# Optimization experiments

Hardware: AMD Instinct MI355X
Metric: run time of the kernel (lower is better)

The kernel has to match this reference:

```python
import jax, jax.numpy as jnp
import numpy as np

TOP_K = 4


def setup_inputs() -> dict:
    key = jax.random.key(0)
    k1, k2, k3 = jax.random.split(key, 3)
    tokens, hidden_dim, num_experts = 16384, 2880, 128
    hidden_states = jax.random.normal(k1, (tokens, hidden_dim), dtype=jnp.float32)
    weight = jax.random.normal(k2, (num_experts, hidden_dim), dtype=jnp.float32) * 0.02
    bias = jax.random.normal(k3, (num_experts,), dtype=jnp.float32) * 0.02
    return {"hidden_states": hidden_states, "weight": weight, "bias": bias}


def reference(hidden_states, weight, bias):
    # hidden_states: [T, H]; weight: [E, H]; bias: [E]
    x = hidden_states.reshape(-1, weight.shape[1])
    router_logits = jnp.einsum("th,eh->te", x, weight) + bias  # [T, E]
    router_top_value, router_indices = jax.lax.top_k(router_logits, TOP_K)  # [T, K]
    router_top_value = jax.nn.softmax(router_top_value, axis=-1)
    return router_top_value, router_indices, router_logits
```

## Files before the change

kernel.cpp:

```cpp
#include <hip/hip_runtime.h>
#include <math.h>

#define H       2880
#define H4      720
#define NTOK    16384
#define NEXP    128
#define NCHUNK  90
#define NSTEP   180
#define GAP_EPS 1e-3f

typedef __attribute__((ext_vector_type(8)))  short bf16x8;
typedef __attribute__((ext_vector_type(16))) float f32x16;

union FragU { unsigned int u[4]; bf16x8 v; };

__device__ inline bf16x8 pack_hi2(float4 a, float4 b) {
    const float f[8] = {a.x,a.y,a.z,a.w,b.x,b.y,b.z,b.w};
    FragU r;
#pragma unroll
    for (int j = 0; j < 4; ++j) {
        unsigned u0 = __float_as_uint(f[2*j]);
        unsigned u1 = __float_as_uint(f[2*j+1]);
        r.u[j] = (u1 & 0xFFFF0000u) | (u0 >> 16);
    }
    return r.v;
}
__device__ inline bf16x8 pack_lo2(float4 a, float4 b) {
    const float f[8] = {a.x,a.y,a.z,a.w,b.x,b.y,b.z,b.w};
    FragU r;
#pragma unroll
    for (int j = 0; j < 4; ++j) {
        float x0 = f[2*j],   h0 = __uint_as_float(__float_as_uint(x0) & 0xFFFF0000u);
        float x1 = f[2*j+1], h1 = __uint_as_float(__float_as_uint(x1) & 0xFFFF0000u);
        unsigned l0 = __float_as_uint(x0 - h0);
        unsigned l1 = __float_as_uint(x1 - h1);
        r.u[j] = (l1 & 0xFFFF0000u) | (l0 >> 16);
    }
    return r.v;
}

__global__ __launch_bounds__(256) void wconv(
    const float* __restrict__ w, short* __restrict__ whiF, short* __restrict__ wloF)
{
    const int gid = blockIdx.x * 256 + threadIdx.x;
    const int l   = gid & 63;
    const int nt  = (gid >> 6) & 3;
    const int s   = gid >> 8;
    const int e   = nt * 32 + (l & 31);
    const int k0  = s * 16 + (l >> 5) * 8;
    const float4* wp = (const float4*)(w + (size_t)e * H + k0);
    const float4 a = wp[0], b = wp[1];
    *(bf16x8*)(whiF + (size_t)gid * 8) = pack_hi2(a, b);
    *(bf16x8*)(wloF + (size_t)gid * 8) = pack_lo2(a, b);
}

__global__ __launch_bounds__(64, 2) void router_gemm_mfma(
    const float* __restrict__ x,
    const short* __restrict__ whiF,
    const short* __restrict__ wloF,
    float* __restrict__ p0,
    float* __restrict__ pws)
{
    __shared__ float xs[3][1024];

    const int lane = threadIdx.x;
    const int bm   = blockIdx.x;
    const int z    = blockIdx.y;
    const int ks   = gridDim.y;
    const int t0   = bm * 32;

    const int base = NCHUNK / ks, rem = NCHUNK % ks;
    const int c0 = z * base + (z < rem ? z : rem);
    const int c1 = c0 + base + (z < rem ? 1 : 0);

    float* outp = (z == 0) ? p0 : (pws + (size_t)(z - 1) * NTOK * NEXP);

    const float4* gs = (const float4*)x + (size_t)(t0 + (lane >> 3)) * H4 + ((lane & 7) ^ (lane >> 3));
    const unsigned xsb = (unsigned)(uintptr_t)&xs[0][0];
    const int r31 = lane & 31, lx7 = lane & 7, kh2 = (lane >> 5) * 2;

    f32x16 acc[4];
#pragma unroll
    for (int nt = 0; nt < 4; ++nt)
#pragma unroll
        for (int r = 0; r < 16; ++r) acc[nt][r] = 0.0f;

    bf16x8 bc[16], bn[16];

#define GL(SRC, DST) __builtin_amdgcn_global_load_lds(                                   \
        (const __attribute__((address_space(1))) void*)(SRC),                            \
        (__attribute__((address_space(3))) void*)(DST), 16, 0, 0)

#define STAGE(SB, CC) {                                                                  \
    const float4* g_ = gs + (size_t)(CC) * 8;                                            \
    GL(g_,                  &xs[SB][0]);                                                 \
    GL(g_ + (size_t) 8*H4,  &xs[SB][256]);                                               \
    GL(g_ + (size_t)16*H4,  &xs[SB][512]);                                               \
    GL(g_ + (size_t)24*H4,  &xs[SB][768]); }

#define BLOAD_ST(DST, CC, ST) {                                                          \
    _Pragma("unroll")                                                                    \
    for (int nt = 0; nt < 4; ++nt) {                                                     \
        const size_t o_ = ((size_t)(((CC)*2 + (ST))*4 + nt)*64 + lane) * 8;              \
        DST[(ST)*8 + nt*2]     = *(const bf16x8*)(whiF + o_);                            \
        DST[(ST)*8 + nt*2 + 1] = *(const bf16x8*)(wloF + o_); } }

#define MFMA_ST(ST, AH, AL) {                                                            \
    _Pragma("unroll")                                                                    \
    for (int nt = 0; nt < 4; ++nt) {                                                     \
        acc[nt] = __builtin_amdgcn_mfma_f32_32x32x16_bf16(AH, bc[(ST)*8 + nt*2],     acc[nt], 0,0,0); \
        acc[nt] = __builtin_amdgcn_mfma_f32_32x32x16_bf16(AL, bc[(ST)*8 + nt*2],     acc[nt], 0,0,0); \
        acc[nt] = __builtin_amdgcn_mfma_f32_32x32x16_bf16(AH, bc[(ST)*8 + nt*2 + 1], acc[nt], 0,0,0); } }

#define BODY(C, DOB) {                                                                   \
    const unsigned ab  = xsb + (unsigned)rb * 4096u + (unsigned)r31 * 128u;              \
    const unsigned a00 = ab + 16u * (unsigned)((kh2    ) ^ lx7);                         \
    const unsigned a01 = ab + 16u * (unsigned)((kh2 + 1) ^ lx7);                         \
    const unsigned a10 = ab + 16u * (unsigned)((kh2 + 4) ^ lx7);                         \
    const unsigned a11 = ab + 16u * (unsigned)((kh2 + 5) ^ lx7);                         \
    float4 q0, q1, q2, q3;                                                               \
    asm volatile("ds_read_b128 %0, %1" : "=v"(q0) : "v"(a00) : "memory");                \
    asm volatile("ds_read_b128 %0, %1" : "=v"(q1) : "v"(a01) : "memory");                \
    asm volatile("ds_read_b128 %0, %1" : "=v"(q2) : "v"(a10) : "memory");                \
    asm volatile("ds_read_b128 %0, %1" : "=v"(q3) : "v"(a11) : "memory");                \
    asm volatile("s_waitcnt lgkmcnt(0)" ::: "memory");                                   \
    __builtin_amdgcn_sched_barrier(0);                                                   \
    const bf16x8 ah0 = pack_hi2(q0, q1), al0 = pack_lo2(q0, q1);                         \
    const bf16x8 ah1 = pack_hi2(q2, q3), al1 = pack_lo2(q2, q3);                         \
    if (DOB) BLOAD_ST(bn, (C) + 1, 0);                                                   \
    MFMA_ST(0, ah0, al0);                                                                \
    if (DOB) BLOAD_ST(bn, (C) + 1, 1);                                                   \
    MFMA_ST(1, ah1, al1);                                                                \
    if (DOB) { _Pragma("unroll") for (int i_ = 0; i_ < 16; ++i_) bc[i_] = bn[i_]; }      \
    rb = (rb == 2) ? 0 : rb + 1; }

#define ITER(C, DOSTAGE, VMSTR, DOB) {                                                   \
    if (DOSTAGE) { STAGE(sb, (C) + 2); sb = (sb == 2) ? 0 : sb + 1; }                    \
    asm volatile("s_waitcnt vmcnt(" VMSTR ")" ::: "memory");                             \
    BODY((C), DOB) }

    int rb = c0 % 3;
    int sb = rb + 2; if (sb >= 3) sb -= 3;
    int b1 = rb + 1; if (b1 >= 3) b1 -= 3;

    STAGE(rb, c0);
    STAGE(b1, c0 + 1);
    BLOAD_ST(bc, c0, 0);
    BLOAD_ST(bc, c0, 1);

    ITER(c0,     true,  "24", true);
    ITER(c0 + 1, true,  "40", true);
    for (int c = c0 + 2; c < c1 - 2; ++c) {
        ITER(c, true, "40", true);
    }
    ITER(c1 - 2, false, "36", true);
    ITER(c1 - 1, false, "32", false);

    const int ecol  = lane & 31;
    const int rbase = t0 + 4 * (lane >> 5);
#pragma unroll
    for (int nt = 0; nt < 4; ++nt)
#pragma unroll
        for (int r = 0; r < 16; ++r) {
            const int orow = rbase + (r & 3) + 8 * (r >> 2);
            outp[(size_t)orow * NEXP + nt * 32 + ecol] = acc[nt][r];
        }
}

__global__ __launch_bounds__(256) void reduce_cand(
    float* __restrict__ p0,
    const float* __restrict__ pws,
    const float* __restrict__ bias,
    int* __restrict__ cand,
    float* __restrict__ vals,
    float* __restrict__ inds,
    int ks)
{
    const int tid = threadIdx.x;
    const int tok = blockIdx.x * 8 + (tid >> 5);
    const int l   = tid & 31;

    float4* row = (float4*)p0 + (size_t)tok * 32 + l;
    float4 s = row[0];
    for (int zz = 1; zz < ks; ++zz) {
        const float4 pz = ((const float4*)(pws + (size_t)(zz - 1) * NTOK * NEXP))[(size_t)tok * 32 + l];
        s.x += pz.x; s.y += pz.y; s.z += pz.z; s.w += pz.w;
    }
    const float4 bb = ((const float4*)bias)[l];
    s.x += bb.x; s.y += bb.y; s.z += bb.z; s.w += bb.w;
    row[0] = s;

    float v[4] = {s.x, s.y, s.z, s.w};
    float vv[8]; int out[8];
#pragma unroll
    for (int r = 0; r < 8; ++r) {
        float lv = v[0]; int lj = 0;
#pragma unroll
        for (int j = 1; j < 4; ++j) if (v[j] > lv) { lv = v[j]; lj = j; }
        int le = l * 4 + lj;
#pragma unroll
        for (int m = 1; m < 32; m <<= 1) {
            const float ov = __shfl_xor(lv, m, 32);
            const int   oe = __shfl_xor(le, m, 32);
            if (ov > lv || (ov == lv && oe < le)) { lv = ov; le = oe; }
        }
        vv[r] = lv; out[r] = le;
        if ((le >> 2) == l) v[le & 3] = -3.4e38f;
    }

    float ming = vv[0] - vv[1];
    ming = fminf(ming, vv[1] - vv[2]);
    ming = fminf(ming, vv[2] - vv[3]);
    ming = fminf(ming, vv[3] - vv[4]);
    const bool slow = (ming < GAP_EPS);

    if (l == 0) {
        int4 o0 = {out[0] | (slow ? (1 << 30) : 0), out[1], out[2], out[3]};
        int4 o1 = {out[4], out[5], out[6], out[7]};
        *(int4*)(cand + (size_t)tok * 8)     = o0;
        *(int4*)(cand + (size_t)tok * 8 + 4) = o1;
        if (!slow) {
            const float e1 = expf(vv[1] - vv[0]);
            const float e2 = expf(vv[2] - vv[0]);
            const float e3 = expf(vv[3] - vv[0]);
            const float sm = 1.0f + e1 + e2 + e3;
            float4 ov = {1.0f / sm, e1 / sm, e2 / sm, e3 / sm};
            float4 oi = {(float)out[0], (float)out[1], (float)out[2], (float)out[3]};
            *(float4*)(&vals[(size_t)tok * 4]) = ov;
            *(float4*)(&inds[(size_t)tok * 4]) = oi;
        }
    }
}

__global__ __launch_bounds__(256) void fixup_topk(
    const float* __restrict__ x,
    const float* __restrict__ w,
    const float* __restrict__ bias,
    const int* __restrict__ cand,
    float* __restrict__ vals,
    float* __restrict__ inds)
{
    const int lane = threadIdx.x & 63;
    const int wv   = threadIdx.x >> 6;
    const int tok  = blockIdx.x * 4 + wv;

    const int head = cand[(size_t)tok * 8];
    if (!(head & (1 << 30))) return;

    const int c    = lane >> 3;
    const int s    = lane & 7;
    const int cidx = cand[(size_t)tok * 8 + c] & 0x3fffffff;

    const float4* xr = (const float4*)x + (size_t)tok  * H4;
    const float4* wr = (const float4*)w + (size_t)cidx * H4;

    double acc = 0.0;
    for (int j = 0; j < 90; ++j) {
        const float4 a = xr[s + 8 * j];
        const float4 b = wr[s + 8 * j];
        acc = fma((double)a.x, (double)b.x, acc);
        acc = fma((double)a.y, (double)b.y, acc);
        acc = fma((double)a.z, (double)b.z, acc);
        acc = fma((double)a.w, (double)b.w, acc);
    }
    acc += __shfl_xor(acc, 1);
    acc += __shfl_xor(acc, 2);
    acc += __shfl_xor(acc, 4);
    const double exact = acc + (double)bias[cidx];

    double bv[8]; int bidx[8];
#pragma unroll
    for (int g = 0; g < 8; ++g) { bv[g] = __shfl(exact, g * 8); bidx[g] = __shfl(cidx, g * 8); }

    float fv[4]; int fi[4];
#pragma unroll
    for (int k = 0; k < 4; ++k) {
        double best = -1.0e300; int bi = 1 << 30; int bg = -1;
#pragma unroll
        for (int g = 0; g < 8; ++g) {
            if (bv[g] > best || (bv[g] == best && bidx[g] < bi)) { best = bv[g]; bi = bidx[g]; bg = g; }
        }
#pragma unroll
        for (int g = 0; g < 8; ++g) if (g == bg) bv[g] = -1.0e300;
        fv[k] = (float)best; fi[k] = bi;
    }

    if (lane == 0) {
        const float e1 = expf(fv[1] - fv[0]);
        const float e2 = expf(fv[2] - fv[0]);
        const float e3 = expf(fv[3] - fv[0]);
        const float sm = 1.0f + e1 + e2 + e3;
        float4 ov = {1.0f / sm, e1 / sm, e2 / sm, e3 / sm};
        float4 oi = {(float)fi[0], (float)fi[1], (float)fi[2], (float)fi[3]};
        *(float4*)(&vals[(size_t)tok * 4]) = ov;
        *(float4*)(&inds[(size_t)tok * 4]) = oi;
    }
}

extern "C" void kernel_launch(void* const* d_in, const int* in_sizes, int n_in,
                              void* d_out, int out_size, void* d_ws, size_t ws_size,
                              hipStream_t stream) {
    const float* x    = (const float*)d_in[0];
    const float* w    = (const float*)d_in[1];
    const float* bias = (const float*)d_in[2];

    float* out    = (float*)d_out;
    float* vals   = out;
    float* inds   = out + NTOK * 4;
    float* logits = out + NTOK * 8;

    const size_t WPLANE = (size_t)NEXP * H * sizeof(short);
    const size_t PB     = (size_t)NTOK * NEXP * sizeof(float);
    const size_t CB     = (size_t)NTOK * 8 * sizeof(int);

    int ks = 1;
    if      (ws_size >= 2 * WPLANE + 3 * PB + CB) ks = 4;
    else if (ws_size >= 2 * WPLANE + 1 * PB + CB) ks = 2;

    short* whiF = (short*)d_ws;
    short* wloF = whiF + (size_t)NEXP * H;
    float* pws  = (float*)(wloF + (size_t)NEXP * H);
    int*   cand = (int*)(pws + (size_t)(ks - 1) * NTOK * NEXP);

    wconv<<<NSTEP, 256, 0, stream>>>(w, whiF, wloF);
    router_gemm_mfma<<<dim3(NTOK / 32, ks), 64, 0, stream>>>(x, whiF, wloF, logits, pws);
    reduce_cand<<<NTOK / 8, 256, 0, stream>>>(logits, pws, bias, cand, vals, inds, ks);
    fixup_topk<<<NTOK / 4, 256, 0, stream>>>(x, w, bias, cand, vals, inds);
}
```

Before: 87.04 us.

## Fuse split-K reduction and top-k into GEMM tail; compact fixup token list

Removes the separate reduce_cand kernel: the last split-K block for each row tile (found with an atomic counter and threadfences) sums the partials, adds the bias and runs the top-k and softmax itself. Tokens whose top-k gap is ambiguous are appended to a compacted list with an atomic counter, so the fixup kernel runs a small persistent grid over only those tokens instead of launching one wave per token. This saves one kernel launch, one full pass over the partials and the wasted fixup waves, at the cost of a memset, serialized tail work in the last block, and atomic contention.

```diff
diff --git a/kernel.cpp b/kernel.cpp
--- a/kernel.cpp
+++ b/kernel.cpp
@@ -59,7 +59,14 @@
     const short* __restrict__ whiF,
     const short* __restrict__ wloF,
     float* __restrict__ p0,
-    float* __restrict__ pws)
+    float* __restrict__ pws,
+    const float* __restrict__ bias,
+    int* __restrict__ cnt,
+    int* __restrict__ nfix,
+    int* __restrict__ list,
+    int* __restrict__ cand,
+    float* __restrict__ vals,
+    float* __restrict__ inds)
 {
     __shared__ float xs[3][1024];
 
@@ -165,69 +172,71 @@
             const int orow = rbase + (r & 3) + 8 * (r >> 2);
             outp[(size_t)orow * NEXP + nt * 32 + ecol] = acc[nt][r];
         }
-}
-
-__global__ __launch_bounds__(256) void reduce_cand(
-    float* __restrict__ p0,
-    const float* __restrict__ pws,
-    const float* __restrict__ bias,
-    int* __restrict__ cand,
-    float* __restrict__ vals,
-    float* __restrict__ inds,
-    int ks)
-{
-    const int tid = threadIdx.x;
-    const int tok = blockIdx.x * 8 + (tid >> 5);
-    const int l   = tid & 31;
-
-    float4* row = (float4*)p0 + (size_t)tok * 32 + l;
-    float4 s = row[0];
-    for (int zz = 1; zz < ks; ++zz) {
-        const float4 pz = ((const float4*)(pws + (size_t)(zz - 1) * NTOK * NEXP))[(size_t)tok * 32 + l];
-        s.x += pz.x; s.y += pz.y; s.z += pz.z; s.w += pz.w;
-    }
+
+    __threadfence();
+    int old = 0;
+    if (lane == 0) old = atomicAdd(&cnt[bm], 1);
+    old = __shfl(old, 0);
+    if (old != ks - 1) return;
+    __threadfence();
+
+    const int l  = lane & 31;
+    const int th = lane >> 5;
     const float4 bb = ((const float4*)bias)[l];
-    s.x += bb.x; s.y += bb.y; s.z += bb.z; s.w += bb.w;
-    row[0] = s;
-
-    float v[4] = {s.x, s.y, s.z, s.w};
-    float vv[8]; int out[8];
-#pragma unroll
-    for (int r = 0; r < 8; ++r) {
-        float lv = v[0]; int lj = 0;
-#pragma unroll
-        for (int j = 1; j < 4; ++j) if (v[j] > lv) { lv = v[j]; lj = j; }
-        int le = l * 4 + lj;
-#pragma unroll
-        for (int m = 1; m < 32; m <<= 1) {
-            const float ov = __shfl_xor(lv, m, 32);
-            const int   oe = __shfl_xor(le, m, 32);
-            if (ov > lv || (ov == lv && oe < le)) { lv = ov; le = oe; }
-        }
-        vv[r] = lv; out[r] = le;
-        if ((le >> 2) == l) v[le & 3] = -3.4e38f;
-    }
-
-    float ming = vv[0] - vv[1];
-    ming = fminf(ming, vv[1] - vv[2]);
-    ming = fminf(ming, vv[2] - vv[3]);
-    ming = fminf(ming, vv[3] - vv[4]);
-    const bool slow = (ming < GAP_EPS);
-
-    if (l == 0) {
-        int4 o0 = {out[0] | (slow ? (1 << 30) : 0), out[1], out[2], out[3]};
-        int4 o1 = {out[4], out[5], out[6], out[7]};
-        *(int4*)(cand + (size_t)tok * 8)     = o0;
-        *(int4*)(cand + (size_t)tok * 8 + 4) = o1;
-        if (!slow) {
-            const float e1 = expf(vv[1] - vv[0]);
-            const float e2 = expf(vv[2] - vv[0]);
-            const float e3 = expf(vv[3] - vv[0]);
-            const float sm = 1.0f + e1 + e2 + e3;
-            float4 ov = {1.0f / sm, e1 / sm, e2 / sm, e3 / sm};
-            float4 oi = {(float)out[0], (float)out[1], (float)out[2], (float)out[3]};
-            *(float4*)(&vals[(size_t)tok * 4]) = ov;
-            *(float4*)(&inds[(size_t)tok * 4]) = oi;
+
+    for (int i = 0; i < 16; ++i) {
+        const int tok = t0 + i * 2 + th;
+        float4* rowp = (float4*)p0 + (size_t)tok * 32 + l;
+        float4 s = *rowp;
+        for (int zz = 1; zz < ks; ++zz) {
+            const float4 pz = ((const float4*)(pws + (size_t)(zz - 1) * NTOK * NEXP))[(size_t)tok * 32 + l];
+            s.x += pz.x; s.y += pz.y; s.z += pz.z; s.w += pz.w;
+        }
+        s.x += bb.x; s.y += bb.y; s.z += bb.z; s.w += bb.w;
+        *rowp = s;
+
+        float v[4] = {s.x, s.y, s.z, s.w};
+        float vv[8]; int out8[8];
+#pragma unroll
+        for (int r = 0; r < 8; ++r) {
+            float lv = v[0]; int lj = 0;
+#pragma unroll
+            for (int j = 1; j < 4; ++j) if (v[j] > lv) { lv = v[j]; lj = j; }
+            int le = l * 4 + lj;
+#pragma unroll
+            for (int m = 1; m < 32; m <<= 1) {
+                const float ov = __shfl_xor(lv, m, 32);
+                const int   oe = __shfl_xor(le, m, 32);
+                if (ov > lv || (ov == lv && oe < le)) { lv = ov; le = oe; }
+            }
+            vv[r] = lv; out8[r] = le;
+            if ((le >> 2) == l) v[le & 3] = -3.4e38f;
+        }
+
+        float ming = vv[0] - vv[1];
+        ming = fminf(ming, vv[1] - vv[2]);
+        ming = fminf(ming, vv[2] - vv[3]);
+        ming = fminf(ming, vv[3] - vv[4]);
+        const bool slow = (ming < GAP_EPS);
+
+        if (l == 0) {
+            if (!slow) {
+                const float e1 = expf(vv[1] - vv[0]);
+                const float e2 = expf(vv[2] - vv[0]);
+                const float e3 = expf(vv[3] - vv[0]);
+                const float sm = 1.0f + e1 + e2 + e3;
+                float4 ov = {1.0f / sm, e1 / sm, e2 / sm, e3 / sm};
+                float4 oi = {(float)out8[0], (float)out8[1], (float)out8[2], (float)out8[3]};
+                *(float4*)(&vals[(size_t)tok * 4]) = ov;
+                *(float4*)(&inds[(size_t)tok * 4]) = oi;
+            } else {
+                int4 o0 = {out8[0], out8[1], out8[2], out8[3]};
+                int4 o1 = {out8[4], out8[5], out8[6], out8[7]};
+                *(int4*)(cand + (size_t)tok * 8)     = o0;
+                *(int4*)(cand + (size_t)tok * 8 + 4) = o1;
+                const int pos = atomicAdd(nfix, 1);
+                list[pos] = tok;
+            }
         }
     }
 }
@@ -236,64 +245,66 @@
     const float* __restrict__ x,
     const float* __restrict__ w,
     const float* __restrict__ bias,
+    const int* __restrict__ nfix,
+    const int* __restrict__ list,
     const int* __restrict__ cand,
     float* __restrict__ vals,
     float* __restrict__ inds)
 {
+    const int wg   = blockIdx.x * 4 + (threadIdx.x >> 6);
     const int lane = threadIdx.x & 63;
-    const int wv   = threadIdx.x >> 6;
-    const int tok  = blockIdx.x * 4 + wv;
-
-    const int head = cand[(size_t)tok * 8];
-    if (!(head & (1 << 30))) return;
-
-    const int c    = lane >> 3;
-    const int s    = lane & 7;
-    const int cidx = cand[(size_t)tok * 8 + c] & 0x3fffffff;
-
-    const float4* xr = (const float4*)x + (size_t)tok  * H4;
-    const float4* wr = (const float4*)w + (size_t)cidx * H4;
-
-    double acc = 0.0;
-    for (int j = 0; j < 90; ++j) {
-        const float4 a = xr[s + 8 * j];
-        const float4 b = wr[s + 8 * j];
-        acc = fma((double)a.x, (double)b.x, acc);
-        acc = fma((double)a.y, (double)b.y, acc);
-        acc = fma((double)a.z, (double)b.z, acc);
-        acc = fma((double)a.w, (double)b.w, acc);
-    }
-    acc += __shfl_xor(acc, 1);
-    acc += __shfl_xor(acc, 2);
-    acc += __shfl_xor(acc, 4);
-    const double exact = acc + (double)bias[cidx];
-
-    double bv[8]; int bidx[8];
-#pragma unroll
-    for (int g = 0; g < 8; ++g) { bv[g] = __shfl(exact, g * 8); bidx[g] = __shfl(cidx, g * 8); }
-
-    float fv[4]; int fi[4];
-#pragma unroll
-    for (int k = 0; k < 4; ++k) {
-        double best = -1.0e300; int bi = 1 << 30; int bg = -1;
-#pragma unroll
-        for (int g = 0; g < 8; ++g) {
-            if (bv[g] > best || (bv[g] == best && bidx[g] < bi)) { best = bv[g]; bi = bidx[g]; bg = g; }
-        }
-#pragma unroll
-        for (int g = 0; g < 8; ++g) if (g == bg) bv[g] = -1.0e300;
-        fv[k] = (float)best; fi[k] = bi;
-    }
-
-    if (lane == 0) {
-        const float e1 = expf(fv[1] - fv[0]);
-        const float e2 = expf(fv[2] - fv[0]);
-        const float e3 = expf(fv[3] - fv[0]);
-        const float sm = 1.0f + e1 + e2 + e3;
-        float4 ov = {1.0f / sm, e1 / sm, e2 / sm, e3 / sm};
-        float4 oi = {(float)fi[0], (float)fi[1], (float)fi[2], (float)fi[3]};
-        *(float4*)(&vals[(size_t)tok * 4]) = ov;
-        *(float4*)(&inds[(size_t)tok * 4]) = oi;
+    const int n    = *nfix;
+
+    for (int ii = wg; ii < n; ii += 1024) {
+        const int tok  = list[ii];
+        const int c    = lane >> 3;
+        const int s    = lane & 7;
+        const int cidx = cand[(size_t)tok * 8 + c];
+
+        const float4* xr = (const float4*)x + (size_t)tok  * H4;
+        const float4* wr = (const float4*)w + (size_t)cidx * H4;
+
+        double acc = 0.0;
+        for (int j = 0; j < 90; ++j) {
+            const float4 a = xr[s + 8 * j];
+            const float4 b = wr[s + 8 * j];
+            acc = fma((double)a.x, (double)b.x, acc);
+            acc = fma((double)a.y, (double)b.y, acc);
+            acc = fma((double)a.z, (double)b.z, acc);
+            acc = fma((double)a.w, (double)b.w, acc);
+        }
+        acc += __shfl_xor(acc, 1);
+        acc += __shfl_xor(acc, 2);
+        acc += __shfl_xor(acc, 4);
+        const double exact = acc + (double)bias[cidx];
+
+        double bv[8]; int bidx[8];
+#pragma unroll
+        for (int g = 0; g < 8; ++g) { bv[g] = __shfl(exact, g * 8); bidx[g] = __shfl(cidx, g * 8); }
+
+        float fv[4]; int fi[4];
+#pragma unroll
+        for (int k = 0; k < 4; ++k) {
+            double best = -1.0e300; int bi = 1 << 30; int bg = -1;
+#pragma unroll
+            for (int g = 0; g < 8; ++g) {
+                if (bv[g] > best || (bv[g] == best && bidx[g] < bi)) { best = bv[g]; bi = bidx[g]; bg = g; }
+            }
+#pragma unroll
+            for (int g = 0; g < 8; ++g) if (g == bg) bv[g] = -1.0e300;
+            fv[k] = (float)best; fi[k] = bi;
+        }
+
+        if (lane == 0) {
+            const float e1 = expf(fv[1] - fv[0]);
+            const float e2 = expf(fv[2] - fv[0]);
+            const float e3 = expf(fv[3] - fv[0]);
+            const float sm = 1.0f + e1 + e2 + e3;
+            float4 ov = {1.0f / sm, e1 / sm, e2 / sm, e3 / sm};
+            float4 oi = {(float)fi[0], (float)fi[1], (float)fi[2], (float)fi[3]};
+            *(float4*)(&vals[(size_t)tok * 4]) = ov;
+            *(float4*)(&inds[(size_t)tok * 4]) = oi;
+        }
     }
 }
 
@@ -311,19 +322,23 @@
 
     const size_t WPLANE = (size_t)NEXP * H * sizeof(short);
     const size_t PB     = (size_t)NTOK * NEXP * sizeof(float);
-    const size_t CB     = (size_t)NTOK * 8 * sizeof(int);
+    const size_t TAIL   = (512 + 1 + NTOK + NTOK * 8) * sizeof(int);
 
     int ks = 1;
-    if      (ws_size >= 2 * WPLANE + 3 * PB + CB) ks = 4;
-    else if (ws_size >= 2 * WPLANE + 1 * PB + CB) ks = 2;
+    if      (ws_size >= 2 * WPLANE + 3 * PB + TAIL) ks = 4;
+    else if (ws_size >= 2 * WPLANE + 1 * PB + TAIL) ks = 2;
 
     short* whiF = (short*)d_ws;
     short* wloF = whiF + (size_t)NEXP * H;
     float* pws  = (float*)(wloF + (size_t)NEXP * H);
-    int*   cand = (int*)(pws + (size_t)(ks - 1) * NTOK * NEXP);
-
+    int*   cnt  = (int*)(pws + (size_t)(ks - 1) * NTOK * NEXP);
+    int*   nfix = cnt + 512;
+    int*   list = nfix + 1;
+    int*   cand = list + NTOK;
+
+    hipMemsetAsync(cnt, 0, 513 * sizeof(int), stream);
     wconv<<<NSTEP, 256, 0, stream>>>(w, whiF, wloF);
-    router_gemm_mfma<<<dim3(NTOK / 32, ks), 64, 0, stream>>>(x, whiF, wloF, logits, pws);
-    reduce_cand<<<NTOK / 8, 256, 0, stream>>>(logits, pws, bias, cand, vals, inds, ks);
-    fixup_topk<<<NTOK / 4, 256, 0, stream>>>(x, w, bias, cand, vals, inds);
-}
+    router_gemm_mfma<<<dim3(NTOK / 32, ks), 64, 0, stream>>>(
+        x, whiF, wloF, logits, pws, bias, cnt, nfix, list, cand, vals, inds);
+    fixup_topk<<<256, 256, 0, stream>>>(x, w, bias, nfix, list, cand, vals, inds);
+}
```

Measured after the change: 233.5 us. 168% more time.

## Double-bank B fragments with 2-chunk unrolled loop, removing register copies

Applied to the files above, without the earlier changes.

Replaces the bc/bn copy-based B prefetch with two register banks, bA and bB, that alternate across a loop unrolled by two chunks. Each bank is reloaded directly after its MFMAs consume it, which removes the 16-register copy per iteration and gives the weight loads a deeper prefetch distance. The split-K chunk assignment is changed so each z-slice gets an even number of chunks to fit the unroll. The cost is higher register pressure and hand-tuned vmcnt counts that must match the new load order.

```diff
diff --git a/kernel.cpp b/kernel.cpp
--- a/kernel.cpp
+++ b/kernel.cpp
@@ -69,9 +69,10 @@
     const int ks   = gridDim.y;
     const int t0   = bm * 32;
 
-    const int base = NCHUNK / ks, rem = NCHUNK % ks;
-    const int c0 = z * base + (z < rem ? z : rem);
-    const int c1 = c0 + base + (z < rem ? 1 : 0);
+    const int base2 = (NCHUNK / ks) & ~1;
+    const int pairs = (NCHUNK - base2 * ks) >> 1;
+    const int c0 = z * base2 + 2 * (z < pairs ? z : pairs);
+    const int c1 = c0 + base2 + (z < pairs ? 2 : 0);
 
     float* outp = (z == 0) ? p0 : (pws + (size_t)(z - 1) * NTOK * NEXP);
 
@@ -85,7 +86,7 @@
 #pragma unroll
         for (int r = 0; r < 16; ++r) acc[nt][r] = 0.0f;
 
-    bf16x8 bc[16], bn[16];
+    bf16x8 bA[16], bB[16];
 
 #define GL(SRC, DST) __builtin_amdgcn_global_load_lds(                                   \
         (const __attribute__((address_space(1))) void*)(SRC),                            \
@@ -105,15 +106,15 @@
         DST[(ST)*8 + nt*2]     = *(const bf16x8*)(whiF + o_);                            \
         DST[(ST)*8 + nt*2 + 1] = *(const bf16x8*)(wloF + o_); } }
 
-#define MFMA_ST(ST, AH, AL) {                                                            \
+#define MFMA_HALF(BANK, ST, AH, AL) {                                                    \
     _Pragma("unroll")                                                                    \
     for (int nt = 0; nt < 4; ++nt) {                                                     \
-        acc[nt] = __builtin_amdgcn_mfma_f32_32x32x16_bf16(AH, bc[(ST)*8 + nt*2],     acc[nt], 0,0,0); \
-        acc[nt] = __builtin_amdgcn_mfma_f32_32x32x16_bf16(AL, bc[(ST)*8 + nt*2],     acc[nt], 0,0,0); \
-        acc[nt] = __builtin_amdgcn_mfma_f32_32x32x16_bf16(AH, bc[(ST)*8 + nt*2 + 1], acc[nt], 0,0,0); } }
-
-#define BODY(C, DOB) {                                                                   \
-    const unsigned ab  = xsb + (unsigned)rb * 4096u + (unsigned)r31 * 128u;              \
+        acc[nt] = __builtin_amdgcn_mfma_f32_32x32x16_bf16(AH, BANK[(ST)*8 + nt*2],     acc[nt], 0,0,0); \
+        acc[nt] = __builtin_amdgcn_mfma_f32_32x32x16_bf16(AL, BANK[(ST)*8 + nt*2],     acc[nt], 0,0,0); \
+        acc[nt] = __builtin_amdgcn_mfma_f32_32x32x16_bf16(AH, BANK[(ST)*8 + nt*2 + 1], acc[nt], 0,0,0); } }
+
+#define DSREAD_PACK(BUF, AH0, AL0, AH1, AL1) {                                           \
+    const unsigned ab  = xsb + (unsigned)(BUF) * 4096u + (unsigned)r31 * 128u;           \
     const unsigned a00 = ab + 16u * (unsigned)((kh2    ) ^ lx7);                         \
     const unsigned a01 = ab + 16u * (unsigned)((kh2 + 1) ^ lx7);                         \
     const unsigned a10 = ab + 16u * (unsigned)((kh2 + 4) ^ lx7);                         \
@@ -125,36 +126,46 @@
     asm volatile("ds_read_b128 %0, %1" : "=v"(q3) : "v"(a11) : "memory");                \
     asm volatile("s_waitcnt lgkmcnt(0)" ::: "memory");                                   \
     __builtin_amdgcn_sched_barrier(0);                                                   \
-    const bf16x8 ah0 = pack_hi2(q0, q1), al0 = pack_lo2(q0, q1);                         \
-    const bf16x8 ah1 = pack_hi2(q2, q3), al1 = pack_lo2(q2, q3);                         \
-    if (DOB) BLOAD_ST(bn, (C) + 1, 0);                                                   \
-    MFMA_ST(0, ah0, al0);                                                                \
-    if (DOB) BLOAD_ST(bn, (C) + 1, 1);                                                   \
-    MFMA_ST(1, ah1, al1);                                                                \
-    if (DOB) { _Pragma("unroll") for (int i_ = 0; i_ < 16; ++i_) bc[i_] = bn[i_]; }      \
-    rb = (rb == 2) ? 0 : rb + 1; }
-
-#define ITER(C, DOSTAGE, VMSTR, DOB) {                                                   \
-    if (DOSTAGE) { STAGE(sb, (C) + 2); sb = (sb == 2) ? 0 : sb + 1; }                    \
-    asm volatile("s_waitcnt vmcnt(" VMSTR ")" ::: "memory");                             \
-    BODY((C), DOB) }
-
-    int rb = c0 % 3;
-    int sb = rb + 2; if (sb >= 3) sb -= 3;
-    int b1 = rb + 1; if (b1 >= 3) b1 -= 3;
-
-    STAGE(rb, c0);
-    STAGE(b1, c0 + 1);
-    BLOAD_ST(bc, c0, 0);
-    BLOAD_ST(bc, c0, 1);
-
-    ITER(c0,     true,  "24", true);
-    ITER(c0 + 1, true,  "40", true);
-    for (int c = c0 + 2; c < c1 - 2; ++c) {
-        ITER(c, true, "40", true);
-    }
-    ITER(c1 - 2, false, "36", true);
-    ITER(c1 - 1, false, "32", false);
+    AH0 = pack_hi2(q0, q1); AL0 = pack_lo2(q0, q1);                                      \
+    AH1 = pack_hi2(q2, q3); AL1 = pack_lo2(q2, q3); }
+
+    STAGE(0, c0);
+    STAGE(1, c0 + 1);
+    BLOAD_ST(bA, c0, 0);     BLOAD_ST(bA, c0, 1);
+    BLOAD_ST(bB, c0 + 1, 0); BLOAD_ST(bB, c0 + 1, 1);
+
+    int rb = 0;
+    bf16x8 ah0, al0, ah1, al1;
+    for (int c = c0; c < c1 - 2; c += 2) {
+        const int sb  = (rb + 2 >= 3) ? rb - 1 : rb + 2;
+        const int rb1 = (rb + 1 >= 3) ? 0 : rb + 1;
+        STAGE(sb, c + 2);
+        asm volatile("s_waitcnt vmcnt(40)" ::: "memory");
+        DSREAD_PACK(rb, ah0, al0, ah1, al1);
+        MFMA_HALF(bA, 0, ah0, al0);
+        BLOAD_ST(bA, c + 2, 0);
+        MFMA_HALF(bA, 1, ah1, al1);
+        BLOAD_ST(bA, c + 2, 1);
+        STAGE(rb, c + 3);
+        asm volatile("s_waitcnt vmcnt(40)" ::: "memory");
+        DSREAD_PACK(rb1, ah0, al0, ah1, al1);
+        MFMA_HALF(bB, 0, ah0, al0);
+        BLOAD_ST(bB, c + 3, 0);
+        MFMA_HALF(bB, 1, ah1, al1);
+        BLOAD_ST(bB, c + 3, 1);
+        rb = (rb >= 1) ? rb - 1 : 2;
+    }
+    {
+        const int rb1 = (rb + 1 >= 3) ? 0 : rb + 1;
+        asm volatile("s_waitcnt vmcnt(36)" ::: "memory");
+        DSREAD_PACK(rb, ah0, al0, ah1, al1);
+        MFMA_HALF(bA, 0, ah0, al0);
+        MFMA_HALF(bA, 1, ah1, al1);
+        asm volatile("s_waitcnt vmcnt(16)" ::: "memory");
+        DSREAD_PACK(rb1, ah0, al0, ah1, al1);
+        MFMA_HALF(bB, 0, ah0, al0);
+        MFMA_HALF(bB, 1, ah1, al1);
+    }
 
     const int ecol  = lane & 31;
     const int rbase = t0 + 4 * (lane >> 5);
```

Result: no change. 85.65 us (-1.6%).
